# Optimization experiments

Measured on AMD Instinct MI355X. Metric: run time of the kernel, lower is better.

The kernel has to match this reference:

```python
import jax, jax.numpy as jnp
import numpy as np

HEAD_NUM = 16
EMBED = 1024

def setup_inputs() -> dict:
    key = jax.random.key(0)
    k1, k2, k3 = jax.random.split(key, 3)
    x = jax.random.normal(k1, (2, 2048, EMBED), dtype=jnp.float32)
    W_qkv = jax.random.normal(k2, (3 * EMBED, EMBED), dtype=jnp.float32) * (EMBED ** -0.5)
    W_out = jax.random.normal(k3, (EMBED, EMBED), dtype=jnp.float32) * (EMBED ** -0.5)
    return {"x": x, "W_qkv": W_qkv, "W_out": W_out}

def reference(x, W_qkv, W_out):
    b, t, E = x.shape
    h = HEAD_NUM
    d = E // h
    dk = (E / h) ** 0.5
    qkv = x @ W_qkv.T  # [b, t, 3E]
    # einops 'b t (d k h) -> k b h t d' with k=3, h=head_num (d outermost in the split)
    qkv = qkv.reshape(b, t, d, 3, h).transpose(3, 0, 4, 1, 2)  # [3, b, h, t, d]
    q, k, v = qkv[0], qkv[1], qkv[2]
    energy = jnp.einsum('bhid,bhjd->bhij', q, k) / dk  # [b, h, t, t]
    attn = jax.nn.softmax(energy, axis=-1)
    out = jnp.einsum('bhij,bhjd->bhid', attn, v)  # [b, h, t, d]
    out = out.transpose(0, 2, 1, 3).reshape(b, t, E)  # 'b h t d -> b t (h d)'
    return out @ W_out.T
```

## Files before the change

### kernel.cpp

```cpp
#include <hip/hip_runtime.h>
#include <hip/hip_bf16.h>


#define HEADS 16
#define EMB   1024
#define HDIM  64
#define BB    2
#define TT    2048
#define QSCALE 0.18033688011112042f

typedef __attribute__((ext_vector_type(8)))  short      bf16x8;
typedef __attribute__((ext_vector_type(8)))  _Float16   f16x8;
typedef __attribute__((ext_vector_type(4)))  float      f32x4;
typedef __attribute__((ext_vector_type(16))) float      f32x16;
typedef __attribute__((ext_vector_type(4)))  unsigned   u32x4;

__device__ __forceinline__ unsigned short f2bf(float f) {
    __hip_bfloat16 h = __float2bfloat16(f);
    return __builtin_bit_cast(unsigned short, h);
}
__device__ __forceinline__ float fexp2(float x) {
#if __has_builtin(__builtin_amdgcn_exp2f)
    return __builtin_amdgcn_exp2f(x);
#else
    return exp2f(x);
#endif
}
__device__ __forceinline__ unsigned pkrtz(float a, float b) {
    auto r = __builtin_amdgcn_cvt_pkrtz(a, b);
    return __builtin_bit_cast(unsigned, r);
}
__device__ __forceinline__ unsigned short f2h(float f) {
    return (unsigned short)(pkrtz(f, 0.f) & 0xffffu);
}
__device__ __forceinline__ float h2f(unsigned short u) {
    return (float)__builtin_bit_cast(_Float16, u);
}
__device__ __forceinline__ void gload_lds16(const void* g, void* l) {
    __builtin_amdgcn_global_load_lds(
        (const __attribute__((address_space(1))) void*)g,
        (__attribute__((address_space(3))) void*)l, 16, 0, 0);
}
__device__ __forceinline__ int swzi(int row, int blk) {
    return row * 64 + ((blk ^ (row & 7)) << 3);
}
__device__ __forceinline__ void pl32swap(unsigned& a, unsigned& b) {
    asm("v_permlane32_swap_b32 %0, %1" : "+v"(a), "+v"(b));
}

__global__ __launch_bounds__(256)
void conv_bf16(const float* __restrict__ src, unsigned short* __restrict__ dst,
               int n8) {
    int i = blockIdx.x * 256 + threadIdx.x;
    if (i >= n8) return;
    const float4 v0 = ((const float4*)src)[i * 2];
    const float4 v1 = ((const float4*)src)[i * 2 + 1];
    ushort4 a, b;
    a.x = f2bf(v0.x); a.y = f2bf(v0.y); a.z = f2bf(v0.z); a.w = f2bf(v0.w);
    b.x = f2bf(v1.x); b.y = f2bf(v1.y); b.z = f2bf(v1.z); b.w = f2bf(v1.w);
    ((ushort4*)dst)[i * 2]     = a;
    ((ushort4*)dst)[i * 2 + 1] = b;
}

template<int PERM>
__global__ __launch_bounds__(256)
void convw(const float* __restrict__ src, unsigned short* __restrict__ dst) {
    const int np = blockIdx.x;
    const int ns = PERM ? ((np & 63) * 48 + (np >> 10) * 16 + ((np >> 6) & 15))
                        : np;
    const float4 v = ((const float4*)(src + (size_t)ns * 1024))[threadIdx.x];
    ushort4 u;
    u.x = f2bf(v.x); u.y = f2bf(v.y); u.z = f2bf(v.z); u.w = f2bf(v.w);
    ((ushort4*)(dst + (size_t)np * 1024))[threadIdx.x] = u;
}

template<int EPI>
__global__ __launch_bounds__(256)
void gemm_bf16(const unsigned short* __restrict__ Ag,
               const unsigned short* __restrict__ Wg,
               float* __restrict__ Cout,
               unsigned short* __restrict__ QKb,
               unsigned short* __restrict__ Vt) {
    __shared__ __align__(16) unsigned short AbL[3][128 * 32];
    __shared__ __align__(16) unsigned short WbL[3][128 * 32];

    const int tid = threadIdx.x, lane = tid & 63, w = tid >> 6;
    const int n0 = blockIdx.x * 128, m0 = blockIdx.y * 128;
    const int wn = (w >> 1) * 64, wm = (w & 1) * 64;
    const int r16 = lane & 15, g = lane >> 4;
    const int goff = ((g ^ ((r16 >> 1) & 3)) << 3);

    f32x4 acc[4][4];
    #pragma unroll
    for (int i = 0; i < 4; ++i)
        #pragma unroll
        for (int j = 0; j < 4; ++j)
            acc[i][j] = (f32x4){0.f, 0.f, 0.f, 0.f};

    const int srow = w * 16 + (lane >> 2);
    const int scol = ((lane & 3) ^ ((lane >> 3) & 3)) << 3;
    const int sdst = (w * 16) * 32;
    const unsigned short* Asrc = Ag + (size_t)(m0 + srow) * 1024 + scol;
    const unsigned short* Wsrc = Wg + (size_t)(n0 + srow) * 1024 + scol;

#define STAGE(AB, WB, K0)                                            \
    do {                                                             \
        gload_lds16(Asrc + (K0),              (AB) + sdst);          \
        gload_lds16(Asrc + (K0) + 64 * 1024,  (AB) + sdst + 2048);   \
        gload_lds16(Wsrc + (K0),              (WB) + sdst);          \
        gload_lds16(Wsrc + (K0) + 64 * 1024,  (WB) + sdst + 2048);   \
    } while (0)

    unsigned short *pa0 = &AbL[0][0], *pa1 = &AbL[1][0], *pa2 = &AbL[2][0];
    unsigned short *pw0 = &WbL[0][0], *pw1 = &WbL[1][0], *pw2 = &WbL[2][0];

    STAGE(pa0, pw0, 0);
    STAGE(pa1, pw1, 32);

    for (int kt = 0; kt < 32; ++kt) {
        if (kt < 31) asm volatile("s_waitcnt vmcnt(4)" ::: "memory");
        else         asm volatile("s_waitcnt vmcnt(0)" ::: "memory");
        __builtin_amdgcn_s_barrier();
        if (kt < 30) STAGE(pa2, pw2, (kt + 2) * 32);

        bf16x8 xf[4];
        #pragma unroll
        for (int mi = 0; mi < 4; ++mi)
            xf[mi] = *(const bf16x8*)&pa0[(wm + mi * 16 + r16) * 32 + goff];
        __builtin_amdgcn_s_setprio(1);
        #pragma unroll
        for (int ni = 0; ni < 4; ++ni) {
            const bf16x8 wf = *(const bf16x8*)&pw0[(wn + ni * 16 + r16) * 32 + goff];
            #pragma unroll
            for (int mi = 0; mi < 4; ++mi)
                acc[ni][mi] = __builtin_amdgcn_mfma_f32_16x16x32_bf16(
                    wf, xf[mi], acc[ni][mi], 0, 0, 0);
        }
        __builtin_amdgcn_s_setprio(0);

        unsigned short* t;
        t = pa0; pa0 = pa1; pa1 = pa2; pa2 = t;
        t = pw0; pw0 = pw1; pw1 = pw2; pw2 = t;
    }
#undef STAGE

    const int gq = g * 4;
    if (EPI == 0) {
        #pragma unroll
        for (int ni = 0; ni < 4; ++ni)
            #pragma unroll
            for (int mi = 0; mi < 4; ++mi) {
                const int m = m0 + wm + mi * 16 + r16;
                *(f32x4*)&Cout[(size_t)m * 1024 + (n0 + wn + ni * 16 + gq)] =
                    acc[ni][mi];
            }
    } else if (n0 < 2048) {
        #pragma unroll
        for (int ni = 0; ni < 4; ++ni) {
            const float qs = (n0 + wn + ni * 16) < 1024 ? QSCALE : 1.0f;
            #pragma unroll
            for (int mi = 0; mi < 4; ++mi) {
                const int m  = m0 + wm + mi * 16 + r16;
                const int np = n0 + wn + ni * 16 + gq;
                ushort4 u;
                u.x = f2bf(acc[ni][mi][0] * qs); u.y = f2bf(acc[ni][mi][1] * qs);
                u.z = f2bf(acc[ni][mi][2] * qs); u.w = f2bf(acc[ni][mi][3] * qs);
                *(ushort4*)&QKb[(size_t)m * 2048 + np] = u;
            }
        }
    } else {
        const int b = m0 >> 11, t0 = m0 & 2047;
        #pragma unroll
        for (int ni = 0; ni < 4; ++ni)
            #pragma unroll
            for (int mi = 0; mi < 4; ++mi) {
                const int t   = t0 + wm + mi * 16 + r16;
                const int nv0 = (n0 - 2048) + wn + ni * 16 + gq;
                #pragma unroll
                for (int j = 0; j < 4; ++j) {
                    const int nv = nv0 + j, h = nv >> 6, d = nv & 63;
                    Vt[(((size_t)(b * HEADS + h)) * HDIM + d) * TT + t] =
                        f2h(acc[ni][mi][j]);
                }
            }
    }
}

__global__ __launch_bounds__(256, 4)
void attn32(const unsigned short* __restrict__ QKb,
            const unsigned short* __restrict__ Vt,
            unsigned short* __restrict__ PO0,
            unsigned short* __restrict__ PO1,
            float* __restrict__ PL0,
            float* __restrict__ PL1) {
    __shared__ __align__(16) unsigned short Ks[2][64 * 64];
    __shared__ __align__(16) unsigned short Vs[2][64 * 64];

    const int tid = threadIdx.x, lane = tid & 63, w = tid >> 6;
    const int l31 = lane & 31, hi = lane >> 5;
    const int qt = blockIdx.x & 15, kh = blockIdx.x >> 4;
    const int h = blockIdx.y, b = blockIdx.z;
    const int kbase = kh * 1024;
    const unsigned short* Vsrc = Vt + (size_t)(b * HEADS + h) * HDIM * TT;
    unsigned short* PO = kh ? PO1 : PO0;
    float*          PL = kh ? PL1 : PL0;

    bf16x8 qf[4];
    {
        const unsigned short* qrow =
            QKb + ((size_t)(b * TT + qt * 128 + w * 32 + l31)) * 2048 + h * HDIM;
        #pragma unroll
        for (int dc = 0; dc < 4; ++dc)
            qf[dc] = *(const bf16x8*)(qrow + dc * 16 + hi * 8);
    }

    const f32x16 zz = {};
    f32x16 o0 = {}, o1 = {};
    float lrun = 0.f;

    const int srl = lane >> 3;
    const int scb = lane & 7;
    const int cbs = (scb ^ srl) << 3;
    const int rl0 = w * 16 + srl;
    const unsigned short* kp0 =
        QKb + (size_t)(b * TT + kbase + rl0) * 2048 + 1024 + h * HDIM + cbs;
    const unsigned short* kp1 = kp0 + (size_t)8 * 2048;
    const unsigned short* vp0 = Vsrc + (size_t)rl0 * TT + kbase + cbs;
    const unsigned short* vp1 = vp0 + (size_t)8 * TT;
    unsigned short* const kd0 = &Ks[0][(w * 16) * 64];
    unsigned short* const kd1 = &Ks[1][(w * 16) * 64];
    unsigned short* const vd0 = &Vs[0][(w * 16) * 64];
    unsigned short* const vd1 = &Vs[1][(w * 16) * 64];

#define STAGE(KD, VD)                                                  \
    do {                                                               \
        gload_lds16(kp0, (KD));        gload_lds16(kp1, (KD) + 512);   \
        gload_lds16(vp0, (VD));        gload_lds16(vp1, (VD) + 512);   \
        kp0 += 64 * 2048; kp1 += 64 * 2048; vp0 += 64; vp1 += 64;      \
    } while (0)

    STAGE(kd0, vd0);

    for (int jt = 0; jt < 16; ++jt) {
        const int bb = jt & 1;
        __syncthreads();
        if (jt < 15) {
            if (bb) STAGE(kd0, vd0); else STAGE(kd1, vd1);
        }
        const unsigned short* KsB = &Ks[bb][0];
        const unsigned short* VsB = &Vs[bb][0];

        f32x16 stA, stB;
        __builtin_amdgcn_s_setprio(1);
        #pragma unroll
        for (int dc = 0; dc < 4; ++dc) {
            const bf16x8 kaA = *(const bf16x8*)&KsB[swzi(l31,      dc * 2 + hi)];
            const bf16x8 kaB = *(const bf16x8*)&KsB[swzi(32 + l31, dc * 2 + hi)];
            if (dc == 0) {
                stA = __builtin_amdgcn_mfma_f32_32x32x16_bf16(kaA, qf[0], zz, 0, 0, 0);
                stB = __builtin_amdgcn_mfma_f32_32x32x16_bf16(kaB, qf[0], zz, 0, 0, 0);
            } else {
                stA = __builtin_amdgcn_mfma_f32_32x32x16_bf16(kaA, qf[dc], stA, 0, 0, 0);
                stB = __builtin_amdgcn_mfma_f32_32x32x16_bf16(kaB, qf[dc], stB, 0, 0, 0);
            }
        }
        __builtin_amdgcn_s_setprio(0);

        #pragma unroll
        for (int x = 0; x < 2; ++x) {
            const f32x16& st = x ? stB : stA;
            float sum;
            unsigned wd[8];
            #pragma unroll
            for (int c = 0; c < 4; ++c) {
                const float e0 = fexp2(st[4 * c + 0]);
                const float e1 = fexp2(st[4 * c + 1]);
                const float e2 = fexp2(st[4 * c + 2]);
                const float e3 = fexp2(st[4 * c + 3]);
                const float s4 = (e0 + e1) + (e2 + e3);
                sum = c ? sum + s4 : s4;
                wd[2 * c]     = pkrtz(e0, e1);
                wd[2 * c + 1] = pkrtz(e2, e3);
            }
            lrun += sum;

            unsigned a0 = wd[0], a2 = wd[2];  pl32swap(a0, a2);
            unsigned a1 = wd[1], a3 = wd[3];  pl32swap(a1, a3);
            unsigned b0 = wd[4], b2 = wd[6];  pl32swap(b0, b2);
            unsigned b1 = wd[5], b3 = wd[7];  pl32swap(b1, b3);
            const u32x4 fa = {a0, a1, a2, a3};
            const u32x4 fb = {b0, b1, b2, b3};
            const f16x8 pa0 = __builtin_bit_cast(f16x8, fa);
            const f16x8 pa1 = __builtin_bit_cast(f16x8, fb);

            const int f0 = 2 * x;
            __builtin_amdgcn_s_setprio(1);
            {
                const f16x8 vb00 = *(const f16x8*)&VsB[swzi(l31,      f0 * 2 + hi)];
                const f16x8 vb01 = *(const f16x8*)&VsB[swzi(32 + l31, f0 * 2 + hi)];
                o0 = __builtin_amdgcn_mfma_f32_32x32x16_f16(pa0, vb00, o0, 0, 0, 0);
                o1 = __builtin_amdgcn_mfma_f32_32x32x16_f16(pa0, vb01, o1, 0, 0, 0);
                const f16x8 vb10 = *(const f16x8*)&VsB[swzi(l31,      (f0 + 1) * 2 + hi)];
                const f16x8 vb11 = *(const f16x8*)&VsB[swzi(32 + l31, (f0 + 1) * 2 + hi)];
                o0 = __builtin_amdgcn_mfma_f32_32x32x16_f16(pa1, vb10, o0, 0, 0, 0);
                o1 = __builtin_amdgcn_mfma_f32_32x32x16_f16(pa1, vb11, o1, 0, 0, 0);
            }
            __builtin_amdgcn_s_setprio(0);
        }
    }
#undef STAGE

    lrun += __shfl_xor(lrun, 32);
    const float inv = 1.0f / lrun;
    #pragma unroll
    for (int r = 0; r < 16; ++r) {
        const int qr = (r & 3) + 8 * (r >> 2) + 4 * hi;
        const float ir = __shfl(inv, qr);
        const int q = qt * 128 + w * 32 + qr;
        unsigned short* dst = PO + ((size_t)(b * TT + q)) * EMB + h * HDIM + l31;
        dst[0]  = f2h(o0[r] * ir);
        dst[32] = f2h(o1[r] * ir);
    }
    if (!hi) {
        const int q = qt * 128 + w * 32 + l31;
        PL[((size_t)(b * HEADS + h)) * TT + q] = lrun;
    }
}

__global__ __launch_bounds__(256)
void merge_attn(const unsigned short* __restrict__ PO0,
                const unsigned short* __restrict__ PO1,
                const float* __restrict__ PL0,
                const float* __restrict__ PL1,
                unsigned short* __restrict__ AOb) {
    const int i = blockIdx.x * 256 + threadIdx.x;
    const int tg  = i >> 8;
    const int col = (i & 255) * 4;
    const int h   = col >> 6;
    const int b   = tg >> 11, t = tg & 2047;

    const float la = PL0[((size_t)(b * HEADS + h)) * TT + t];
    const float lb = PL1[((size_t)(b * HEADS + h)) * TT + t];
    const float inv = 1.0f / (la + lb);
    const float wa = la * inv, wb = lb * inv;

    const ushort4 a = ((const ushort4*)PO0)[i];
    const ushort4 c = ((const ushort4*)PO1)[i];
    ushort4 o;
    o.x = f2bf(h2f(a.x) * wa + h2f(c.x) * wb);
    o.y = f2bf(h2f(a.y) * wa + h2f(c.y) * wb);
    o.z = f2bf(h2f(a.z) * wa + h2f(c.z) * wb);
    o.w = f2bf(h2f(a.w) * wa + h2f(c.w) * wb);
    ((ushort4*)AOb)[i] = o;
}

extern "C" void kernel_launch(void* const* d_in, const int* in_sizes, int n_in,
                              void* d_out, int out_size, void* d_ws, size_t ws_size,
                              hipStream_t stream) {
    const float* x    = (const float*)d_in[0];
    const float* Wqkv = (const float*)d_in[1];
    const float* Wout = (const float*)d_in[2];
    float* out = (float*)d_out;

    unsigned short* Wqb = (unsigned short*)d_ws;
    unsigned short* Wob = Wqb + 3145728;
    unsigned short* xb  = Wob + 1048576;
    unsigned short* QKb = xb  + 4194304;
    unsigned short* Vt  = QKb + 8388608;
    unsigned short* PO0 = Vt  + 4194304;
    unsigned short* PO1 = PO0 + 4194304;
    float*          PL0 = (float*)(PO1 + 4194304);
    float*          PL1 = PL0 + 65536;
    unsigned short* AOb = xb;

    conv_bf16<<<2048, 256, 0, stream>>>(x, xb, 524288);
    convw<1><<<3072, 256, 0, stream>>>(Wqkv, Wqb);
    convw<0><<<1024, 256, 0, stream>>>(Wout, Wob);

    gemm_bf16<1><<<dim3(24, 32), 256, 0, stream>>>(xb, Wqb, nullptr, QKb, Vt);

    attn32<<<dim3(32, 16, 2), 256, 0, stream>>>(QKb, Vt, PO0, PO1, PL0, PL1);

    merge_attn<<<4096, 256, 0, stream>>>(PO0, PO1, PL0, PL1, AOb);

    gemm_bf16<0><<<dim3(8, 32), 256, 0, stream>>>(AOb, Wob, out, nullptr, nullptr);
}
```

Measured before the change: 135.2 us.

## Merge conversion kernels, remap attention blocks, unroll loop with split accumulators

The three fp32-to-bf16 conversion launches are merged into a single launch with branch-per-block-range, removing two kernel launch overheads. The attention kernel remaps block IDs so consecutive blocks spread across XCDs (bid&7 striding), changing L2 locality of K/V reuse across heads. The key-tile loop is unrolled by two with compile-time buffer indices, and PV accumulation is split into two independent accumulator chains per output to break MFMA dependency stalls, at the cost of extra accumulator registers (occupancy pressure with 4 blocks/SM bound).

```diff
diff --git a/kernel.cpp b/kernel.cpp
--- a/kernel.cpp
+++ b/kernel.cpp
@@ -49,29 +49,33 @@
 }
 
 __global__ __launch_bounds__(256)
-void conv_bf16(const float* __restrict__ src, unsigned short* __restrict__ dst,
-               int n8) {
-    int i = blockIdx.x * 256 + threadIdx.x;
-    if (i >= n8) return;
-    const float4 v0 = ((const float4*)src)[i * 2];
-    const float4 v1 = ((const float4*)src)[i * 2 + 1];
-    ushort4 a, b;
-    a.x = f2bf(v0.x); a.y = f2bf(v0.y); a.z = f2bf(v0.z); a.w = f2bf(v0.w);
-    b.x = f2bf(v1.x); b.y = f2bf(v1.y); b.z = f2bf(v1.z); b.w = f2bf(v1.w);
-    ((ushort4*)dst)[i * 2]     = a;
-    ((ushort4*)dst)[i * 2 + 1] = b;
-}
-
-template<int PERM>
-__global__ __launch_bounds__(256)
-void convw(const float* __restrict__ src, unsigned short* __restrict__ dst) {
-    const int np = blockIdx.x;
-    const int ns = PERM ? ((np & 63) * 48 + (np >> 10) * 16 + ((np >> 6) & 15))
-                        : np;
-    const float4 v = ((const float4*)(src + (size_t)ns * 1024))[threadIdx.x];
-    ushort4 u;
-    u.x = f2bf(v.x); u.y = f2bf(v.y); u.z = f2bf(v.z); u.w = f2bf(v.w);
-    ((ushort4*)(dst + (size_t)np * 1024))[threadIdx.x] = u;
+void conv_all(const float* __restrict__ x,    unsigned short* __restrict__ xb,
+              const float* __restrict__ Wqkv, unsigned short* __restrict__ Wqb,
+              const float* __restrict__ Wout, unsigned short* __restrict__ Wob) {
+    const int blk = blockIdx.x;
+    if (blk < 2048) {
+        const int i = blk * 256 + threadIdx.x;
+        const float4 v0 = ((const float4*)x)[i * 2];
+        const float4 v1 = ((const float4*)x)[i * 2 + 1];
+        ushort4 a, b;
+        a.x = f2bf(v0.x); a.y = f2bf(v0.y); a.z = f2bf(v0.z); a.w = f2bf(v0.w);
+        b.x = f2bf(v1.x); b.y = f2bf(v1.y); b.z = f2bf(v1.z); b.w = f2bf(v1.w);
+        ((ushort4*)xb)[i * 2]     = a;
+        ((ushort4*)xb)[i * 2 + 1] = b;
+    } else if (blk < 5120) {
+        const int np = blk - 2048;
+        const int ns = (np & 63) * 48 + (np >> 10) * 16 + ((np >> 6) & 15);
+        const float4 v = ((const float4*)(Wqkv + (size_t)ns * 1024))[threadIdx.x];
+        ushort4 u;
+        u.x = f2bf(v.x); u.y = f2bf(v.y); u.z = f2bf(v.z); u.w = f2bf(v.w);
+        ((ushort4*)(Wqb + (size_t)np * 1024))[threadIdx.x] = u;
+    } else {
+        const int np = blk - 5120;
+        const float4 v = ((const float4*)(Wout + (size_t)np * 1024))[threadIdx.x];
+        ushort4 u;
+        u.x = f2bf(v.x); u.y = f2bf(v.y); u.z = f2bf(v.z); u.w = f2bf(v.w);
+        ((ushort4*)(Wob + (size_t)np * 1024))[threadIdx.x] = u;
+    }
 }
 
 template<int EPI>
@@ -198,8 +202,10 @@
 
     const int tid = threadIdx.x, lane = tid & 63, w = tid >> 6;
     const int l31 = lane & 31, hi = lane >> 5;
-    const int qt = blockIdx.x & 15, kh = blockIdx.x >> 4;
-    const int h = blockIdx.y, b = blockIdx.z;
+    const int bid = blockIdx.x + 32 * blockIdx.y + 512 * blockIdx.z;
+    const int vb  = (bid & 7) * 128 + (bid >> 3);
+    const int qt  = vb & 15, kh = (vb >> 4) & 1;
+    const int h   = (vb >> 5) & 15, b = vb >> 9;
     const int kbase = kh * 1024;
     const unsigned short* Vsrc = Vt + (size_t)(b * HEADS + h) * HDIM * TT;
     unsigned short* PO = kh ? PO1 : PO0;
@@ -215,7 +221,7 @@
     }
 
     const f32x16 zz = {};
-    f32x16 o0 = {}, o1 = {};
+    f32x16 o0a = {}, o0b = {}, o1a = {}, o1b = {};
     float lrun = 0.f;
 
     const int srl = lane >> 3;
@@ -239,76 +245,79 @@
         kp0 += 64 * 2048; kp1 += 64 * 2048; vp0 += 64; vp1 += 64;      \
     } while (0)
 
+#define TILE(BUFI, DOSTAGE)                                                     \
+    do {                                                                        \
+        __syncthreads();                                                        \
+        if (DOSTAGE) { if (BUFI) STAGE(kd0, vd0); else STAGE(kd1, vd1); }       \
+        const unsigned short* KsB = &Ks[BUFI][0];                               \
+        const unsigned short* VsB = &Vs[BUFI][0];                               \
+        f32x16 stA, stB;                                                        \
+        __builtin_amdgcn_s_setprio(1);                                          \
+        _Pragma("unroll")                                                       \
+        for (int dc = 0; dc < 4; ++dc) {                                        \
+            const bf16x8 kaA = *(const bf16x8*)&KsB[swzi(l31,      dc * 2 + hi)]; \
+            const bf16x8 kaB = *(const bf16x8*)&KsB[swzi(32 + l31, dc * 2 + hi)]; \
+            if (dc == 0) {                                                      \
+                stA = __builtin_amdgcn_mfma_f32_32x32x16_bf16(kaA, qf[0], zz, 0, 0, 0); \
+                stB = __builtin_amdgcn_mfma_f32_32x32x16_bf16(kaB, qf[0], zz, 0, 0, 0); \
+            } else {                                                            \
+                stA = __builtin_amdgcn_mfma_f32_32x32x16_bf16(kaA, qf[dc], stA, 0, 0, 0); \
+                stB = __builtin_amdgcn_mfma_f32_32x32x16_bf16(kaB, qf[dc], stB, 0, 0, 0); \
+            }                                                                   \
+        }                                                                       \
+        __builtin_amdgcn_s_setprio(0);                                          \
+        _Pragma("unroll")                                                       \
+        for (int x = 0; x < 2; ++x) {                                           \
+            const f32x16& st = x ? stB : stA;                                   \
+            float sum;                                                          \
+            unsigned wd[8];                                                     \
+            _Pragma("unroll")                                                   \
+            for (int c = 0; c < 4; ++c) {                                       \
+                const float e0 = fexp2(st[4 * c + 0]);                          \
+                const float e1 = fexp2(st[4 * c + 1]);                          \
+                const float e2 = fexp2(st[4 * c + 2]);                          \
+                const float e3 = fexp2(st[4 * c + 3]);                          \
+                const float s4 = (e0 + e1) + (e2 + e3);                         \
+                sum = c ? sum + s4 : s4;                                        \
+                wd[2 * c]     = pkrtz(e0, e1);                                  \
+                wd[2 * c + 1] = pkrtz(e2, e3);                                  \
+            }                                                                   \
+            lrun += sum;                                                        \
+            unsigned a0 = wd[0], a2 = wd[2];  pl32swap(a0, a2);                 \
+            unsigned a1 = wd[1], a3 = wd[3];  pl32swap(a1, a3);                 \
+            unsigned b0 = wd[4], b2 = wd[6];  pl32swap(b0, b2);                 \
+            unsigned b1 = wd[5], b3 = wd[7];  pl32swap(b1, b3);                 \
+            const u32x4 fva = {a0, a1, a2, a3};                                 \
+            const u32x4 fvb = {b0, b1, b2, b3};                                 \
+            const f16x8 pa0 = __builtin_bit_cast(f16x8, fva);                   \
+            const f16x8 pa1 = __builtin_bit_cast(f16x8, fvb);                   \
+            const int f0 = 2 * x;                                               \
+            __builtin_amdgcn_s_setprio(1);                                      \
+            {                                                                   \
+                const f16x8 vb00 = *(const f16x8*)&VsB[swzi(l31,      f0 * 2 + hi)]; \
+                const f16x8 vb01 = *(const f16x8*)&VsB[swzi(32 + l31, f0 * 2 + hi)]; \
+                o0a = __builtin_amdgcn_mfma_f32_32x32x16_f16(pa0, vb00, o0a, 0, 0, 0); \
+                o1a = __builtin_amdgcn_mfma_f32_32x32x16_f16(pa0, vb01, o1a, 0, 0, 0); \
+                const f16x8 vb10 = *(const f16x8*)&VsB[swzi(l31,      (f0 + 1) * 2 + hi)]; \
+                const f16x8 vb11 = *(const f16x8*)&VsB[swzi(32 + l31, (f0 + 1) * 2 + hi)]; \
+                o0b = __builtin_amdgcn_mfma_f32_32x32x16_f16(pa1, vb10, o0b, 0, 0, 0); \
+                o1b = __builtin_amdgcn_mfma_f32_32x32x16_f16(pa1, vb11, o1b, 0, 0, 0); \
+            }                                                                   \
+            __builtin_amdgcn_s_setprio(0);                                      \
+        }                                                                       \
+    } while (0)
+
     STAGE(kd0, vd0);
 
-    for (int jt = 0; jt < 16; ++jt) {
-        const int bb = jt & 1;
-        __syncthreads();
-        if (jt < 15) {
-            if (bb) STAGE(kd0, vd0); else STAGE(kd1, vd1);
-        }
-        const unsigned short* KsB = &Ks[bb][0];
-        const unsigned short* VsB = &Vs[bb][0];
-
-        f32x16 stA, stB;
-        __builtin_amdgcn_s_setprio(1);
-        #pragma unroll
-        for (int dc = 0; dc < 4; ++dc) {
-            const bf16x8 kaA = *(const bf16x8*)&KsB[swzi(l31,      dc * 2 + hi)];
-            const bf16x8 kaB = *(const bf16x8*)&KsB[swzi(32 + l31, dc * 2 + hi)];
-            if (dc == 0) {
-                stA = __builtin_amdgcn_mfma_f32_32x32x16_bf16(kaA, qf[0], zz, 0, 0, 0);
-                stB = __builtin_amdgcn_mfma_f32_32x32x16_bf16(kaB, qf[0], zz, 0, 0, 0);
-            } else {
-                stA = __builtin_amdgcn_mfma_f32_32x32x16_bf16(kaA, qf[dc], stA, 0, 0, 0);
-                stB = __builtin_amdgcn_mfma_f32_32x32x16_bf16(kaB, qf[dc], stB, 0, 0, 0);
-            }
-        }
-        __builtin_amdgcn_s_setprio(0);
-
-        #pragma unroll
-        for (int x = 0; x < 2; ++x) {
-            const f32x16& st = x ? stB : stA;
-            float sum;
-            unsigned wd[8];
-            #pragma unroll
-            for (int c = 0; c < 4; ++c) {
-                const float e0 = fexp2(st[4 * c + 0]);
-                const float e1 = fexp2(st[4 * c + 1]);
-                const float e2 = fexp2(st[4 * c + 2]);
-                const float e3 = fexp2(st[4 * c + 3]);
-                const float s4 = (e0 + e1) + (e2 + e3);
-                sum = c ? sum + s4 : s4;
-                wd[2 * c]     = pkrtz(e0, e1);
-                wd[2 * c + 1] = pkrtz(e2, e3);
-            }
-            lrun += sum;
-
-            unsigned a0 = wd[0], a2 = wd[2];  pl32swap(a0, a2);
-            unsigned a1 = wd[1], a3 = wd[3];  pl32swap(a1, a3);
-            unsigned b0 = wd[4], b2 = wd[6];  pl32swap(b0, b2);
-            unsigned b1 = wd[5], b3 = wd[7];  pl32swap(b1, b3);
-            const u32x4 fa = {a0, a1, a2, a3};
-            const u32x4 fb = {b0, b1, b2, b3};
-            const f16x8 pa0 = __builtin_bit_cast(f16x8, fa);
-            const f16x8 pa1 = __builtin_bit_cast(f16x8, fb);
-
-            const int f0 = 2 * x;
-            __builtin_amdgcn_s_setprio(1);
-            {
-                const f16x8 vb00 = *(const f16x8*)&VsB[swzi(l31,      f0 * 2 + hi)];
-                const f16x8 vb01 = *(const f16x8*)&VsB[swzi(32 + l31, f0 * 2 + hi)];
-                o0 = __builtin_amdgcn_mfma_f32_32x32x16_f16(pa0, vb00, o0, 0, 0, 0);
-                o1 = __builtin_amdgcn_mfma_f32_32x32x16_f16(pa0, vb01, o1, 0, 0, 0);
-                const f16x8 vb10 = *(const f16x8*)&VsB[swzi(l31,      (f0 + 1) * 2 + hi)];
-                const f16x8 vb11 = *(const f16x8*)&VsB[swzi(32 + l31, (f0 + 1) * 2 + hi)];
-                o0 = __builtin_amdgcn_mfma_f32_32x32x16_f16(pa1, vb10, o0, 0, 0, 0);
-                o1 = __builtin_amdgcn_mfma_f32_32x32x16_f16(pa1, vb11, o1, 0, 0, 0);
-            }
-            __builtin_amdgcn_s_setprio(0);
-        }
-    }
+    for (int jt = 0; jt < 16; jt += 2) {
+        TILE(0, true);
+        TILE(1, jt < 14);
+    }
+#undef TILE
 #undef STAGE
+
+    const f32x16 o0 = o0a + o0b;
+    const f32x16 o1 = o1a + o1b;
 
     lrun += __shfl_xor(lrun, 32);
     const float inv = 1.0f / lrun;
@@ -373,9 +382,7 @@
     float*          PL1 = PL0 + 65536;
     unsigned short* AOb = xb;
 
-    conv_bf16<<<2048, 256, 0, stream>>>(x, xb, 524288);
-    convw<1><<<3072, 256, 0, stream>>>(Wqkv, Wqb);
-    convw<0><<<1024, 256, 0, stream>>>(Wout, Wob);
+    conv_all<<<6144, 256, 0, stream>>>(x, xb, Wqkv, Wqb, Wout, Wob);
 
     gemm_bf16<1><<<dim3(24, 32), 256, 0, stream>>>(xb, Wqb, nullptr, QKb, Vt);
 
```

Result: slower. 165.6 us (+22.5%).

## Fuse conversion kernels, remap attention block order, split PV accumulators

Applied to the files above, without the earlier changes.

Merges the three fp32-to-bf16 conversion launches into one kernel that dispatches on block index, removing two launch gaps. Remaps the attention block index so that consecutive blocks spread across heads and batches, which changes XCD and cache locality. Splits each PV accumulator into two independent chains to break the MFMA dependency and summed them at the end, at the cost of more accumulator registers under a 4-wave occupancy bound.

```diff
diff --git a/kernel.cpp b/kernel.cpp
--- a/kernel.cpp
+++ b/kernel.cpp
@@ -49,29 +49,33 @@
 }
 
 __global__ __launch_bounds__(256)
-void conv_bf16(const float* __restrict__ src, unsigned short* __restrict__ dst,
-               int n8) {
-    int i = blockIdx.x * 256 + threadIdx.x;
-    if (i >= n8) return;
-    const float4 v0 = ((const float4*)src)[i * 2];
-    const float4 v1 = ((const float4*)src)[i * 2 + 1];
-    ushort4 a, b;
-    a.x = f2bf(v0.x); a.y = f2bf(v0.y); a.z = f2bf(v0.z); a.w = f2bf(v0.w);
-    b.x = f2bf(v1.x); b.y = f2bf(v1.y); b.z = f2bf(v1.z); b.w = f2bf(v1.w);
-    ((ushort4*)dst)[i * 2]     = a;
-    ((ushort4*)dst)[i * 2 + 1] = b;
-}
-
-template<int PERM>
-__global__ __launch_bounds__(256)
-void convw(const float* __restrict__ src, unsigned short* __restrict__ dst) {
-    const int np = blockIdx.x;
-    const int ns = PERM ? ((np & 63) * 48 + (np >> 10) * 16 + ((np >> 6) & 15))
-                        : np;
-    const float4 v = ((const float4*)(src + (size_t)ns * 1024))[threadIdx.x];
-    ushort4 u;
-    u.x = f2bf(v.x); u.y = f2bf(v.y); u.z = f2bf(v.z); u.w = f2bf(v.w);
-    ((ushort4*)(dst + (size_t)np * 1024))[threadIdx.x] = u;
+void conv_all(const float* __restrict__ x,    unsigned short* __restrict__ xb,
+              const float* __restrict__ Wqkv, unsigned short* __restrict__ Wqb,
+              const float* __restrict__ Wout, unsigned short* __restrict__ Wob) {
+    const int blk = blockIdx.x;
+    if (blk < 2048) {
+        const int i = blk * 256 + threadIdx.x;
+        const float4 v0 = ((const float4*)x)[i * 2];
+        const float4 v1 = ((const float4*)x)[i * 2 + 1];
+        ushort4 a, b;
+        a.x = f2bf(v0.x); a.y = f2bf(v0.y); a.z = f2bf(v0.z); a.w = f2bf(v0.w);
+        b.x = f2bf(v1.x); b.y = f2bf(v1.y); b.z = f2bf(v1.z); b.w = f2bf(v1.w);
+        ((ushort4*)xb)[i * 2]     = a;
+        ((ushort4*)xb)[i * 2 + 1] = b;
+    } else if (blk < 5120) {
+        const int np = blk - 2048;
+        const int ns = (np & 63) * 48 + (np >> 10) * 16 + ((np >> 6) & 15);
+        const float4 v = ((const float4*)(Wqkv + (size_t)ns * 1024))[threadIdx.x];
+        ushort4 u;
+        u.x = f2bf(v.x); u.y = f2bf(v.y); u.z = f2bf(v.z); u.w = f2bf(v.w);
+        ((ushort4*)(Wqb + (size_t)np * 1024))[threadIdx.x] = u;
+    } else {
+        const int np = blk - 5120;
+        const float4 v = ((const float4*)(Wout + (size_t)np * 1024))[threadIdx.x];
+        ushort4 u;
+        u.x = f2bf(v.x); u.y = f2bf(v.y); u.z = f2bf(v.z); u.w = f2bf(v.w);
+        ((ushort4*)(Wob + (size_t)np * 1024))[threadIdx.x] = u;
+    }
 }
 
 template<int EPI>
@@ -198,8 +202,10 @@
 
     const int tid = threadIdx.x, lane = tid & 63, w = tid >> 6;
     const int l31 = lane & 31, hi = lane >> 5;
-    const int qt = blockIdx.x & 15, kh = blockIdx.x >> 4;
-    const int h = blockIdx.y, b = blockIdx.z;
+    const int bid = blockIdx.x + 32 * blockIdx.y + 512 * blockIdx.z;
+    const int vb  = (bid & 7) * 128 + (bid >> 3);
+    const int qt  = vb & 15, kh = (vb >> 4) & 1;
+    const int h   = (vb >> 5) & 15, b = vb >> 9;
     const int kbase = kh * 1024;
     const unsigned short* Vsrc = Vt + (size_t)(b * HEADS + h) * HDIM * TT;
     unsigned short* PO = kh ? PO1 : PO0;
@@ -215,7 +221,7 @@
     }
 
     const f32x16 zz = {};
-    f32x16 o0 = {}, o1 = {};
+    f32x16 o0a = {}, o0b = {}, o1a = {}, o1b = {};
     float lrun = 0.f;
 
     const int srl = lane >> 3;
@@ -288,27 +294,30 @@
             unsigned a1 = wd[1], a3 = wd[3];  pl32swap(a1, a3);
             unsigned b0 = wd[4], b2 = wd[6];  pl32swap(b0, b2);
             unsigned b1 = wd[5], b3 = wd[7];  pl32swap(b1, b3);
-            const u32x4 fa = {a0, a1, a2, a3};
-            const u32x4 fb = {b0, b1, b2, b3};
-            const f16x8 pa0 = __builtin_bit_cast(f16x8, fa);
-            const f16x8 pa1 = __builtin_bit_cast(f16x8, fb);
+            const u32x4 fva = {a0, a1, a2, a3};
+            const u32x4 fvb = {b0, b1, b2, b3};
+            const f16x8 pa0 = __builtin_bit_cast(f16x8, fva);
+            const f16x8 pa1 = __builtin_bit_cast(f16x8, fvb);
 
             const int f0 = 2 * x;
             __builtin_amdgcn_s_setprio(1);
             {
                 const f16x8 vb00 = *(const f16x8*)&VsB[swzi(l31,      f0 * 2 + hi)];
                 const f16x8 vb01 = *(const f16x8*)&VsB[swzi(32 + l31, f0 * 2 + hi)];
-                o0 = __builtin_amdgcn_mfma_f32_32x32x16_f16(pa0, vb00, o0, 0, 0, 0);
-                o1 = __builtin_amdgcn_mfma_f32_32x32x16_f16(pa0, vb01, o1, 0, 0, 0);
+                o0a = __builtin_amdgcn_mfma_f32_32x32x16_f16(pa0, vb00, o0a, 0, 0, 0);
+                o1a = __builtin_amdgcn_mfma_f32_32x32x16_f16(pa0, vb01, o1a, 0, 0, 0);
                 const f16x8 vb10 = *(const f16x8*)&VsB[swzi(l31,      (f0 + 1) * 2 + hi)];
                 const f16x8 vb11 = *(const f16x8*)&VsB[swzi(32 + l31, (f0 + 1) * 2 + hi)];
-                o0 = __builtin_amdgcn_mfma_f32_32x32x16_f16(pa1, vb10, o0, 0, 0, 0);
-                o1 = __builtin_amdgcn_mfma_f32_32x32x16_f16(pa1, vb11, o1, 0, 0, 0);
+                o0b = __builtin_amdgcn_mfma_f32_32x32x16_f16(pa1, vb10, o0b, 0, 0, 0);
+                o1b = __builtin_amdgcn_mfma_f32_32x32x16_f16(pa1, vb11, o1b, 0, 0, 0);
             }
             __builtin_amdgcn_s_setprio(0);
         }
     }
 #undef STAGE
+
+    const f32x16 o0 = o0a + o0b;
+    const f32x16 o1 = o1a + o1b;
 
     lrun += __shfl_xor(lrun, 32);
     const float inv = 1.0f / lrun;
@@ -373,9 +382,7 @@
     float*          PL1 = PL0 + 65536;
     unsigned short* AOb = xb;
 
-    conv_bf16<<<2048, 256, 0, stream>>>(x, xb, 524288);
-    convw<1><<<3072, 256, 0, stream>>>(Wqkv, Wqb);
-    convw<0><<<1024, 256, 0, stream>>>(Wout, Wob);
+    conv_all<<<6144, 256, 0, stream>>>(x, xb, Wqkv, Wqb, Wout, Wob);
 
     gemm_bf16<1><<<dim3(24, 32), 256, 0, stream>>>(xb, Wqb, nullptr, QKb, Vt);
 
```

Result: no change. 137.4 us (+1.7%).
